# Optimization experiments

Measured on AMD Instinct MI355X. Metric: run time of the kernel, lower is better.

Reference implementation:

```python
import jax, jax.numpy as jnp
import numpy as np

H = 4096          # hidden_size
HS = 64           # head_size
NH = H // HS      # num_heads = 64
TM = 64           # TIME_MIX_EXTRA_DIM (hidden_size == 4096)
TD = 128          # TIME_DECAY_EXTRA_DIM (hidden_size == 4096)
EPS = 1e-5


def _ln(v, w, b):
    mu = v.mean(-1, keepdims=True)
    var = v.var(-1, keepdims=True)
    return (v - mu) / jnp.sqrt(var + EPS) * w + b


def setup_inputs() -> dict:
    key = jax.random.key(0)
    ks = jax.random.split(key, 20)
    def n(i, shape, s=0.02):
        return jax.random.normal(ks[i], shape, dtype=jnp.float32) * s
    return {
        "x": n(0, (1, 1, H), 1.0),
        "state1": n(1, (1, 1, H), 1.0),
        "state2": n(2, (NH, HS, HS), 1.0),
        "ln1_w": jnp.ones((H,), jnp.float32),
        "ln1_b": jnp.zeros((H,), jnp.float32),
        "time_maa_x": n(3, (1, 1, H), 0.1),
        "time_maa": n(4, (5, 1, H), 0.1),       # stacked [w,k,v,r,g] mixes
        "maa_w1": n(5, (H, 5 * TM)),
        "maa_w2": n(6, (5, TM, H)),
        "time_decay": n(7, (NH, HS, 1), 0.5),
        "time_first": n(8, (NH, HS, 1), 0.5),
        "decay_w1": n(9, (H, TD)),
        "decay_w2": n(10, (TD, H)),
        "Wr": n(11, (H, H)),
        "Wk": n(12, (H, H)),
        "Wv": n(13, (H, H)),
        "Wg": n(14, (H, H)),
        "Wo": n(15, (H, H)),
        "lnx_w": jnp.ones((H,), jnp.float32),
        "lnx_b": jnp.zeros((H,), jnp.float32),
    }


def reference(x, state1, state2, ln1_w, ln1_b, time_maa_x, time_maa,
              maa_w1, maa_w2, time_decay, time_first, decay_w1, decay_w2,
              Wr, Wk, Wv, Wg, Wo, lnx_w, lnx_b):
    last_x = x
    xl = _ln(x, ln1_w, ln1_b)                         # [1,1,H]
    sx = state1 - xl                                  # token-shift delta
    xxx = xl + sx * time_maa_x                        # [1,1,H]
    xxx = jnp.tanh(xxx @ maa_w1).reshape(5, 1, TM)    # LoRA down, 5 mixes
    xxx = jnp.einsum('fot,fth->foh', xxx, maa_w2)     # LoRA up -> [5,1,H]
    xxx = xl + sx * (xxx + time_maa)                  # [5,1,H]
    mw, mk, mv, mr, mg = xxx[0], xxx[1], xxx[2], xxx[3], xxx[4]  # each [1,H]

    r = (mr @ Wr.T).reshape(NH, 1, HS)
    k = (mk @ Wk.T).reshape(NH, HS, 1)
    v = (mv @ Wv.T).reshape(NH, 1, HS)
    g = jax.nn.silu(mg @ Wg.T)                        # [1,H]

    # data-dependent decay (LoRA): exp(-exp(clip(w)))
    td = (jnp.tanh(mw @ decay_w1) @ decay_w2).reshape(NH, HS, 1) + time_decay
    td = jnp.exp(-jnp.exp(jnp.clip(td, -9.72, 2.27)))

    kv = k @ v                                        # [NH,HS,HS] outer product
    wkv = kv * time_first + state2                    # bonus + state
    out_h = (r @ wkv).reshape(NH, HS)                 # per-head readout
    state2_out = kv + state2 * td                     # state recurrence

    # InstanceNorm2d over head_size per head (no affine), then elementwise affine
    mu = out_h.mean(-1, keepdims=True)
    var = out_h.var(-1, keepdims=True)
    o = ((out_h - mu) / jnp.sqrt(var + EPS)).reshape(1, 1, H)
    o = o * lnx_w + lnx_b
    o = (o * g) @ Wo.T
    return (last_x + o, xl, state2_out)
```

## Files before the change

### kernel.cpp

```cpp
#include <hip/hip_runtime.h>
#include <hip/hip_bf16.h>


#define HDIM 4096
#define NHEAD 64
#define HSZ 64

#define WS_XL    0
#define WS_SX    4096
#define WS_XXX   8192
#define WS_MV    12288
#define WS_PART  32768
#define WS_DPART 32768
#define WS_TD    53248
#define WS_R     57344
#define WS_K     61440
#define WS_V     65536
#define WS_G     69632
#define WS_OG    73728
#define WS_FLAG  77824

typedef unsigned short bfraw;

__device__ __forceinline__ float bf2f(bfraw u) {
    union { unsigned int u; float f; } v; v.u = ((unsigned int)u) << 16; return v.f;
}
__device__ __forceinline__ bfraw f2bf(float f) {
    union { float f; unsigned int u; } v; v.f = f;
    unsigned int u = v.u;
    unsigned int r = (u + 0x7fffu + ((u >> 16) & 1u)) >> 16;
    return (bfraw)r;
}
__device__ __forceinline__ float ldin(const void* p, long long i, bool isbf) {
    return isbf ? bf2f(((const bfraw*)p)[i]) : ((const float*)p)[i];
}
__device__ __forceinline__ void stout(void* p, long long i, float v, bool isbf) {
    if (isbf) ((bfraw*)p)[i] = f2bf(v); else ((float*)p)[i] = v;
}
__device__ __forceinline__ float waveReduce(float v) {
    for (int m = 32; m; m >>= 1) v += __shfl_xor(v, m);
    return v;
}

__global__ __launch_bounds__(256)
void k1_ln_mix(const void* __restrict__ x, const void* __restrict__ st1,
               const void* __restrict__ lnw, const void* __restrict__ lnb,
               const void* __restrict__ tmx, void* __restrict__ dout,
               float* __restrict__ ws) {
    int tid = threadIdx.x;
    __shared__ float red[8];
    __shared__ float sflag;
    {
        const bfraw* p = (const bfraw*)x;
        bfraw u = p[tid];
        int e = (u >> 7) & 0xFF;
        int cnt = (e >= 96 && e <= 144) ? 1 : 0;
        for (int m = 32; m; m >>= 1) cnt += __shfl_xor(cnt, m);
        if ((tid & 63) == 0) red[tid >> 6] = (float)cnt;
        __syncthreads();
        if (tid == 0) {
            float c = red[0] + red[1] + red[2] + red[3];
            float fl = (c >= 208.0f) ? 1.0f : 0.0f;
            sflag = fl;
            ws[WS_FLAG] = fl;
        }
        __syncthreads();
    }
    bool isbf = sflag != 0.0f;

    float xv[16];
    float s1 = 0.f, s2 = 0.f;
    for (int k = 0; k < 16; ++k) {
        float v = ldin(x, tid + k * 256, isbf);
        xv[k] = v; s1 += v; s2 += v * v;
    }
    s1 = waveReduce(s1); s2 = waveReduce(s2);
    int wid = tid >> 6, lane = tid & 63;
    if (lane == 0) { red[wid] = s1; red[4 + wid] = s2; }
    __syncthreads();
    float t1 = red[0] + red[1] + red[2] + red[3];
    float t2 = red[4] + red[5] + red[6] + red[7];
    float mu = t1 * (1.0f / HDIM);
    float var = fmaxf(t2 * (1.0f / HDIM) - mu * mu, 0.0f);
    float rstd = rsqrtf(var + 1e-5f);
    for (int k = 0; k < 16; ++k) {
        int i = tid + k * 256;
        float xl = (xv[k] - mu) * rstd * ldin(lnw, i, isbf) + ldin(lnb, i, isbf);
        float sx = ldin(st1, i, isbf) - xl;
        float xxx = xl + sx * ldin(tmx, i, isbf);
        stout(dout, 4096 + i, xl, isbf);
        ws[WS_XL + i] = xl;
        ws[WS_SX + i] = sx;
        ws[WS_XXX + i] = xxx;
    }
}

__global__ __launch_bounds__(320)
void k2a_maa_down(const void* __restrict__ w1, float* __restrict__ ws) {
    bool isbf = ws[WS_FLAG] != 0.0f;
    __shared__ float lx[64];
    int tid = threadIdx.x, b = blockIdx.x;
    if (tid < 64) lx[tid] = ws[WS_XXX + b * 64 + tid];
    __syncthreads();
    float acc = 0.f;
    long long base = (long long)b * 64 * 320 + tid;
    #pragma unroll 8
    for (int j = 0; j < 64; ++j) acc += lx[j] * ldin(w1, base + (long long)j * 320, isbf);
    ws[WS_PART + b * 320 + tid] = acc;
}

__global__ __launch_bounds__(256)
void k2c_maa_up(const void* __restrict__ w2, const void* __restrict__ tm,
                float* __restrict__ ws) {
    bool isbf = ws[WS_FLAG] != 0.0f;
    int tid = threadIdx.x;
    int f = blockIdx.x >> 4;
    int hb = (blockIdx.x & 15) << 8;
    __shared__ float zl[64];
    if (tid < 64) {
        float s = 0.f;
        #pragma unroll 8
        for (int b = 0; b < 64; ++b) s += ws[WS_PART + b * 320 + f * 64 + tid];
        zl[tid] = tanhf(s);
    }
    __syncthreads();
    int h = hb + tid;
    float acc = 0.f;
    long long base = (long long)f * 64 * HDIM + h;
    #pragma unroll 8
    for (int t = 0; t < 64; ++t) acc += zl[t] * ldin(w2, base + (long long)t * HDIM, isbf);
    float mval = ws[WS_XL + h] + ws[WS_SX + h] * (acc + ldin(tm, f * HDIM + h, isbf));
    ws[WS_MV + f * HDIM + h] = mval;
}

__global__ __launch_bounds__(128)
void k3a_decay_down(const void* __restrict__ dw1, float* __restrict__ ws) {
    bool isbf = ws[WS_FLAG] != 0.0f;
    __shared__ float lm[32];
    int tid = threadIdx.x, b = blockIdx.x;
    if (tid < 32) lm[tid] = ws[WS_MV + b * 32 + tid];
    __syncthreads();
    float acc = 0.f;
    long long base = (long long)b * 32 * 128 + tid;
    #pragma unroll 8
    for (int j = 0; j < 32; ++j) acc += lm[j] * ldin(dw1, base + (long long)j * 128, isbf);
    ws[WS_DPART + b * 128 + tid] = acc;
}

__global__ __launch_bounds__(128)
void k3b_decay_up(const void* __restrict__ dw2, const void* __restrict__ tdec,
                  float* __restrict__ ws) {
    bool isbf = ws[WS_FLAG] != 0.0f;
    int tid = threadIdx.x;
    __shared__ float dz[128];
    {
        float s = 0.f;
        #pragma unroll 8
        for (int b = 0; b < 128; ++b) s += ws[WS_DPART + b * 128 + tid];
        dz[tid] = tanhf(s);
    }
    __syncthreads();
    int i = blockIdx.x * 128 + tid;
    float acc = 0.f;
    #pragma unroll 8
    for (int t = 0; t < 128; ++t) acc += dz[t] * ldin(dw2, (long long)t * HDIM + i, isbf);
    float tv = acc + ldin(tdec, i, isbf);
    tv = fminf(fmaxf(tv, -9.72f), 2.27f);
    ws[WS_TD + i] = expf(-expf(tv));
}

__device__ __forceinline__ float dot_row_lds(const void* __restrict__ W, long long row,
                                             const float* __restrict__ mLds,
                                             int lane, bool isbf) {
    float acc = 0.f;
    if (isbf) {
        const bfraw* wr = (const bfraw*)W + row * HDIM;
        uint4 wv[8];
        #pragma unroll
        for (int it = 0; it < 8; ++it)
            wv[it] = *(const uint4*)(wr + it * 512 + lane * 8);
        __builtin_amdgcn_sched_barrier(0);
        #pragma unroll
        for (int it = 0; it < 8; ++it) {
            int base = it * 512 + lane * 8;
            float4 m0 = *(const float4*)(mLds + base);
            float4 m1 = *(const float4*)(mLds + base + 4);
            uint4 w4 = wv[it];
            acc += bf2f((bfraw)(w4.x & 0xffff)) * m0.x + bf2f((bfraw)(w4.x >> 16)) * m0.y;
            acc += bf2f((bfraw)(w4.y & 0xffff)) * m0.z + bf2f((bfraw)(w4.y >> 16)) * m0.w;
            acc += bf2f((bfraw)(w4.z & 0xffff)) * m1.x + bf2f((bfraw)(w4.z >> 16)) * m1.y;
            acc += bf2f((bfraw)(w4.w & 0xffff)) * m1.z + bf2f((bfraw)(w4.w >> 16)) * m1.w;
        }
    } else {
        const float* wr = (const float*)W + row * HDIM;
        #pragma unroll
        for (int h = 0; h < 2; ++h) {
            float4 av[8];
            #pragma unroll
            for (int it = 0; it < 8; ++it)
                av[it] = *(const float4*)(wr + h * 2048 + it * 256 + lane * 4);
            __builtin_amdgcn_sched_barrier(0);
            #pragma unroll
            for (int it = 0; it < 8; ++it) {
                int base = h * 2048 + it * 256 + lane * 4;
                float4 m0 = *(const float4*)(mLds + base);
                float4 a = av[it];
                acc += a.x * m0.x + a.y * m0.y + a.z * m0.z + a.w * m0.w;
            }
        }
    }
    return waveReduce(acc);
}

__global__ __launch_bounds__(256)
void k4_matvec4(const void* __restrict__ Wr, const void* __restrict__ Wk,
                const void* __restrict__ Wv, const void* __restrict__ Wg,
                float* __restrict__ ws) {
    bool isbf = ws[WS_FLAG] != 0.0f;
    int tid = threadIdx.x;
    int wid = tid >> 6, lane = tid & 63;
    int mat = blockIdx.x >> 9;
    int bb = blockIdx.x & 511;
    int bs = (bb & 7) * 64 + (bb >> 3);
    const void* W; const float* msrc; float* y;
    if (mat == 0)      { W = Wr; msrc = ws + WS_MV + 3 * HDIM; y = ws + WS_R; }
    else if (mat == 1) { W = Wk; msrc = ws + WS_MV + 1 * HDIM; y = ws + WS_K; }
    else if (mat == 2) { W = Wv; msrc = ws + WS_MV + 2 * HDIM; y = ws + WS_V; }
    else               { W = Wg; msrc = ws + WS_MV + 4 * HDIM; y = ws + WS_G; }
    __shared__ __align__(16) float lm[HDIM];
    for (int i = tid * 4; i < HDIM; i += 1024)
        *(float4*)(lm + i) = *(const float4*)(msrc + i);
    __syncthreads();
    #pragma unroll
    for (int k = 0; k < 2; ++k) {
        int row = bs * 4 + wid + k * 2048;
        float acc = dot_row_lds(W, row, lm, lane, isbf);
        if (lane == 0) {
            if (mat == 3) acc = acc / (1.0f + expf(-acc));
            y[row] = acc;
        }
    }
}

__global__ __launch_bounds__(64)
void k5_heads(const void* __restrict__ state2, const void* __restrict__ tfirst,
              const void* __restrict__ lnxw, const void* __restrict__ lnxb,
              void* __restrict__ dout, float* __restrict__ ws) {
    bool isbf = ws[WS_FLAG] != 0.0f;
    int h = blockIdx.x, j = threadIdx.x;
    int gi = h * 64 + j;
    float rj = ws[WS_R + gi], kj = ws[WS_K + gi], vj = ws[WS_V + gi];
    float tdj = ws[WS_TD + gi];
    float tfj = ldin(tfirst, gi, isbf);
    __shared__ float lr[64], lk[64], ltd[64];
    lr[j] = rj; lk[j] = kj; ltd[j] = tdj;
    float c = waveReduce(rj * kj * tfj);
    __syncthreads();
    float acc = 0.f;
    long long sbase = (long long)h * 4096 + j;
    #pragma unroll 8
    for (int i = 0; i < 64; ++i) {
        float s = ldin(state2, sbase + i * 64, isbf);
        acc += lr[i] * s;
        stout(dout, 8192 + sbase + i * 64, lk[i] * vj + s * ltd[i], isbf);
    }
    float oh = vj * c + acc;
    float s1 = waveReduce(oh);
    float s2 = waveReduce(oh * oh);
    float mu = s1 * (1.0f / 64.0f);
    float var = fmaxf(s2 * (1.0f / 64.0f) - mu * mu, 0.0f);
    float rstd = rsqrtf(var + 1e-5f);
    float o = (oh - mu) * rstd * ldin(lnxw, gi, isbf) + ldin(lnxb, gi, isbf);
    ws[WS_OG + gi] = o * ws[WS_G + gi];
}

__global__ __launch_bounds__(256)
void k6_out(const void* __restrict__ Wo, const void* __restrict__ x,
            void* __restrict__ dout, float* __restrict__ ws) {
    bool isbf = ws[WS_FLAG] != 0.0f;
    int tid = threadIdx.x;
    int wid = tid >> 6, lane = tid & 63;
    int bb = blockIdx.x;
    int bs = (bb & 7) * 64 + (bb >> 3);
    __shared__ __align__(16) float lm[HDIM];
    for (int i = tid * 4; i < HDIM; i += 1024)
        *(float4*)(lm + i) = *(const float4*)(ws + WS_OG + i);
    __syncthreads();
    #pragma unroll
    for (int k = 0; k < 2; ++k) {
        int row = bs * 4 + wid + k * 2048;
        float acc = dot_row_lds(Wo, row, lm, lane, isbf);
        if (lane == 0) stout(dout, row, ldin(x, row, isbf) + acc, isbf);
    }
}

extern "C" void kernel_launch(void* const* d_in, const int* in_sizes, int n_in,
                              void* d_out, int out_size, void* d_ws, size_t ws_size,
                              hipStream_t stream) {
    const void* x      = d_in[0];
    const void* st1    = d_in[1];
    const void* st2    = d_in[2];
    const void* ln1w   = d_in[3];
    const void* ln1b   = d_in[4];
    const void* tmx    = d_in[5];
    const void* tmaa   = d_in[6];
    const void* maw1   = d_in[7];
    const void* maw2   = d_in[8];
    const void* tdec   = d_in[9];
    const void* tfirst = d_in[10];
    const void* dw1    = d_in[11];
    const void* dw2    = d_in[12];
    const void* Wr     = d_in[13];
    const void* Wk     = d_in[14];
    const void* Wv     = d_in[15];
    const void* Wg     = d_in[16];
    const void* Wo     = d_in[17];
    const void* lnxw   = d_in[18];
    const void* lnxb   = d_in[19];

    float* ws = (float*)d_ws;

    k1_ln_mix<<<1, 256, 0, stream>>>(x, st1, ln1w, ln1b, tmx, d_out, ws);
    k2a_maa_down<<<64, 320, 0, stream>>>(maw1, ws);
    k2c_maa_up<<<80, 256, 0, stream>>>(maw2, tmaa, ws);
    k3a_decay_down<<<128, 128, 0, stream>>>(dw1, ws);
    k3b_decay_up<<<32, 128, 0, stream>>>(dw2, tdec, ws);
    k4_matvec4<<<2048, 256, 0, stream>>>(Wr, Wk, Wv, Wg, ws);
    k5_heads<<<64, 64, 0, stream>>>(st2, tfirst, lnxw, lnxb, d_out, ws);
    k6_out<<<512, 256, 0, stream>>>(Wo, x, d_out, ws);
}
```

Baseline: 416.4 us.

## Double-buffer weight row loads in matvec kernels with contiguous rows per wave

The Wr/Wk/Wv/Wg matvec now gives each wave four consecutive rows and software-pipelines their bf16 loads through two register buffers, so the next row's loads are in flight while the current row is consumed. The grid is halved to 1024 blocks, with each block covering 16 contiguous rows instead of the old strided interleaving. The output projection likewise issues loads for two contiguous rows before consuming either. The goal is more memory-level parallelism per wave and less launch overhead, at the cost of higher register pressure and fewer blocks.

```diff
diff --git a/kernel.cpp b/kernel.cpp
--- a/kernel.cpp
+++ b/kernel.cpp
@@ -169,47 +169,47 @@
     ws[WS_TD + i] = expf(-expf(tv));
 }
 
-__device__ __forceinline__ float dot_row_lds(const void* __restrict__ W, long long row,
-                                             const float* __restrict__ mLds,
-                                             int lane, bool isbf) {
-    float acc = 0.f;
-    if (isbf) {
-        const bfraw* wr = (const bfraw*)W + row * HDIM;
-        uint4 wv[8];
+__device__ __forceinline__ void issue8(const bfraw* __restrict__ wr, int lane,
+                                       uint4 buf[8]) {
+    #pragma unroll
+    for (int it = 0; it < 8; ++it)
+        buf[it] = *(const uint4*)(wr + it * 512 + lane * 8);
+}
+__device__ __forceinline__ float consume8(const uint4 buf[8],
+                                          const float* __restrict__ mLds, int lane) {
+    float acc = 0.f;
+    #pragma unroll
+    for (int it = 0; it < 8; ++it) {
+        int base = it * 512 + lane * 8;
+        float4 m0 = *(const float4*)(mLds + base);
+        float4 m1 = *(const float4*)(mLds + base + 4);
+        uint4 w4 = buf[it];
+        acc += bf2f((bfraw)(w4.x & 0xffff)) * m0.x + bf2f((bfraw)(w4.x >> 16)) * m0.y;
+        acc += bf2f((bfraw)(w4.y & 0xffff)) * m0.z + bf2f((bfraw)(w4.y >> 16)) * m0.w;
+        acc += bf2f((bfraw)(w4.z & 0xffff)) * m1.x + bf2f((bfraw)(w4.z >> 16)) * m1.y;
+        acc += bf2f((bfraw)(w4.w & 0xffff)) * m1.z + bf2f((bfraw)(w4.w >> 16)) * m1.w;
+    }
+    return acc;
+}
+__device__ __forceinline__ float dot_row_f32(const float* __restrict__ wr,
+                                             const float* __restrict__ mLds, int lane) {
+    float acc = 0.f;
+    #pragma unroll
+    for (int h = 0; h < 2; ++h) {
+        float4 av[8];
         #pragma unroll
         for (int it = 0; it < 8; ++it)
-            wv[it] = *(const uint4*)(wr + it * 512 + lane * 8);
+            av[it] = *(const float4*)(wr + h * 2048 + it * 256 + lane * 4);
         __builtin_amdgcn_sched_barrier(0);
         #pragma unroll
         for (int it = 0; it < 8; ++it) {
-            int base = it * 512 + lane * 8;
+            int base = h * 2048 + it * 256 + lane * 4;
             float4 m0 = *(const float4*)(mLds + base);
-            float4 m1 = *(const float4*)(mLds + base + 4);
-            uint4 w4 = wv[it];
-            acc += bf2f((bfraw)(w4.x & 0xffff)) * m0.x + bf2f((bfraw)(w4.x >> 16)) * m0.y;
-            acc += bf2f((bfraw)(w4.y & 0xffff)) * m0.z + bf2f((bfraw)(w4.y >> 16)) * m0.w;
-            acc += bf2f((bfraw)(w4.z & 0xffff)) * m1.x + bf2f((bfraw)(w4.z >> 16)) * m1.y;
-            acc += bf2f((bfraw)(w4.w & 0xffff)) * m1.z + bf2f((bfraw)(w4.w >> 16)) * m1.w;
+            float4 a = av[it];
+            acc += a.x * m0.x + a.y * m0.y + a.z * m0.z + a.w * m0.w;
         }
-    } else {
-        const float* wr = (const float*)W + row * HDIM;
-        #pragma unroll
-        for (int h = 0; h < 2; ++h) {
-            float4 av[8];
-            #pragma unroll
-            for (int it = 0; it < 8; ++it)
-                av[it] = *(const float4*)(wr + h * 2048 + it * 256 + lane * 4);
-            __builtin_amdgcn_sched_barrier(0);
-            #pragma unroll
-            for (int it = 0; it < 8; ++it) {
-                int base = h * 2048 + it * 256 + lane * 4;
-                float4 m0 = *(const float4*)(mLds + base);
-                float4 a = av[it];
-                acc += a.x * m0.x + a.y * m0.y + a.z * m0.z + a.w * m0.w;
-            }
-        }
-    }
-    return waveReduce(acc);
+    }
+    return acc;
 }
 
 __global__ __launch_bounds__(256)
@@ -219,9 +219,8 @@
     bool isbf = ws[WS_FLAG] != 0.0f;
     int tid = threadIdx.x;
     int wid = tid >> 6, lane = tid & 63;
-    int mat = blockIdx.x >> 9;
-    int bb = blockIdx.x & 511;
-    int bs = (bb & 7) * 64 + (bb >> 3);
+    int mat = blockIdx.x >> 8;
+    int bb = blockIdx.x & 255;
     const void* W; const float* msrc; float* y;
     if (mat == 0)      { W = Wr; msrc = ws + WS_MV + 3 * HDIM; y = ws + WS_R; }
     else if (mat == 1) { W = Wk; msrc = ws + WS_MV + 1 * HDIM; y = ws + WS_K; }
@@ -231,14 +230,39 @@
     for (int i = tid * 4; i < HDIM; i += 1024)
         *(float4*)(lm + i) = *(const float4*)(msrc + i);
     __syncthreads();
-    #pragma unroll
-    for (int k = 0; k < 2; ++k) {
-        int row = bs * 4 + wid + k * 2048;
-        float acc = dot_row_lds(W, row, lm, lane, isbf);
-        if (lane == 0) {
-            if (mat == 3) acc = acc / (1.0f + expf(-acc));
-            y[row] = acc;
+    int r0 = bb * 16 + wid * 4;
+    float acc0, acc1, acc2, acc3;
+    if (isbf) {
+        const bfraw* w0 = (const bfraw*)W + (long long)r0 * HDIM;
+        uint4 A[8], B[8];
+        issue8(w0, lane, A);
+        issue8(w0 + HDIM, lane, B);
+        __builtin_amdgcn_sched_barrier(0);
+        acc0 = consume8(A, lm, lane);
+        issue8(w0 + 2 * HDIM, lane, A);
+        __builtin_amdgcn_sched_barrier(0);
+        acc1 = consume8(B, lm, lane);
+        issue8(w0 + 3 * HDIM, lane, B);
+        __builtin_amdgcn_sched_barrier(0);
+        acc2 = consume8(A, lm, lane);
+        acc3 = consume8(B, lm, lane);
+    } else {
+        const float* w0 = (const float*)W + (long long)r0 * HDIM;
+        acc0 = dot_row_f32(w0, lm, lane);
+        acc1 = dot_row_f32(w0 + HDIM, lm, lane);
+        acc2 = dot_row_f32(w0 + 2 * HDIM, lm, lane);
+        acc3 = dot_row_f32(w0 + 3 * HDIM, lm, lane);
+    }
+    acc0 = waveReduce(acc0); acc1 = waveReduce(acc1);
+    acc2 = waveReduce(acc2); acc3 = waveReduce(acc3);
+    if (lane == 0) {
+        if (mat == 3) {
+            acc0 = acc0 / (1.0f + expf(-acc0));
+            acc1 = acc1 / (1.0f + expf(-acc1));
+            acc2 = acc2 / (1.0f + expf(-acc2));
+            acc3 = acc3 / (1.0f + expf(-acc3));
         }
+        y[r0] = acc0; y[r0 + 1] = acc1; y[r0 + 2] = acc2; y[r0 + 3] = acc3;
     }
 }
 
@@ -280,17 +304,29 @@
     bool isbf = ws[WS_FLAG] != 0.0f;
     int tid = threadIdx.x;
     int wid = tid >> 6, lane = tid & 63;
-    int bb = blockIdx.x;
-    int bs = (bb & 7) * 64 + (bb >> 3);
     __shared__ __align__(16) float lm[HDIM];
     for (int i = tid * 4; i < HDIM; i += 1024)
         *(float4*)(lm + i) = *(const float4*)(ws + WS_OG + i);
     __syncthreads();
-    #pragma unroll
-    for (int k = 0; k < 2; ++k) {
-        int row = bs * 4 + wid + k * 2048;
-        float acc = dot_row_lds(Wo, row, lm, lane, isbf);
-        if (lane == 0) stout(dout, row, ldin(x, row, isbf) + acc, isbf);
+    int r0 = blockIdx.x * 8 + wid * 2;
+    float acc0, acc1;
+    if (isbf) {
+        const bfraw* w0 = (const bfraw*)Wo + (long long)r0 * HDIM;
+        uint4 A[8], B[8];
+        issue8(w0, lane, A);
+        issue8(w0 + HDIM, lane, B);
+        __builtin_amdgcn_sched_barrier(0);
+        acc0 = consume8(A, lm, lane);
+        acc1 = consume8(B, lm, lane);
+    } else {
+        const float* w0 = (const float*)Wo + (long long)r0 * HDIM;
+        acc0 = dot_row_f32(w0, lm, lane);
+        acc1 = dot_row_f32(w0 + HDIM, lm, lane);
+    }
+    acc0 = waveReduce(acc0); acc1 = waveReduce(acc1);
+    if (lane == 0) {
+        stout(dout, r0,     ldin(x, r0, isbf)     + acc0, isbf);
+        stout(dout, r0 + 1, ldin(x, r0 + 1, isbf) + acc1, isbf);
     }
 }
 
@@ -325,7 +361,7 @@
     k2c_maa_up<<<80, 256, 0, stream>>>(maw2, tmaa, ws);
     k3a_decay_down<<<128, 128, 0, stream>>>(dw1, ws);
     k3b_decay_up<<<32, 128, 0, stream>>>(dw2, tdec, ws);
-    k4_matvec4<<<2048, 256, 0, stream>>>(Wr, Wk, Wv, Wg, ws);
+    k4_matvec4<<<1024, 256, 0, stream>>>(Wr, Wk, Wv, Wg, ws);
     k5_heads<<<64, 64, 0, stream>>>(st2, tfirst, lnxw, lnxb, d_out, ws);
     k6_out<<<512, 256, 0, stream>>>(Wo, x, d_out, ws);
 }
```

New measurement: 418.2 us. Within noise of the previous version (+0.4%).
